# Performance work log

Measured on AMD Instinct MI355X. Metric: run time of the kernel, lower is better.

The kernel has to match this reference:

```python
import jax, jax.numpy as jnp
import numpy as np
from math import sqrt

B, S, I, H, O, R = 32, 2048, 128, 512, 64, 1
ALPHA = 0.1


def setup_inputs() -> dict:
    key = jax.random.key(0)
    ks = jax.random.split(key, 7)
    x = jax.random.normal(ks[0], (B, S, I), dtype=jnp.float32)
    input_projective = jax.random.normal(ks[1], (H, R), dtype=jnp.float32) / sqrt(H)
    input_receptive = jax.random.normal(ks[2], (I, R), dtype=jnp.float32) / sqrt(I)
    rec_projective = jax.random.normal(ks[3], (H, R), dtype=jnp.float32) / sqrt(H)
    rec_receptive = jax.random.normal(ks[4], (H, R), dtype=jnp.float32) / sqrt(H)
    bound = 1.0 / sqrt(H)
    readout_w = jax.random.uniform(ks[5], (O, H), minval=-bound, maxval=bound, dtype=jnp.float32)
    readout_b = jax.random.uniform(ks[6], (O,), minval=-bound, maxval=bound, dtype=jnp.float32)
    return {
        "x": x,
        "input_projective": input_projective,
        "input_receptive": input_receptive,
        "rec_projective": rec_projective,
        "rec_receptive": rec_receptive,
        "readout_w": readout_w,
        "readout_b": readout_b,
    }


def reference(x, input_projective, input_receptive, rec_projective, rec_receptive, readout_w, readout_b):
    # Precompute input drive for all steps using the low-rank factorization:
    # x_in[b,s,h] = x[b,s,:] @ input_receptive @ input_projective.T
    x_in = jnp.einsum("bsi,ir,hr->bsh", x, input_receptive, input_projective)

    def step(h, xin_t):
        # r_in = (J @ h.T).T with J = P @ R.T  ->  h @ R @ P.T (low-rank)
        r_in = (h @ rec_receptive) @ rec_projective.T
        dh = -h + jax.nn.relu(r_in + xin_t)  # activation = nlfun (relu)
        h = h + ALPHA * dh                   # Euler hidden update
        out_t = h @ readout_w.T + readout_b
        return h, out_t

    h0 = jnp.zeros((x.shape[0], rec_projective.shape[0]), dtype=x.dtype)
    _, out = jax.lax.scan(step, h0, jnp.swapaxes(x_in, 0, 1))  # scan over time
    return jnp.swapaxes(out, 0, 1)  # [B, S, O]
```

## Files before the change

### kernel.cpp

```cpp
#include <hip/hip_runtime.h>


#define B_ 32
#define S_ 2048
#define I_ 128
#define H_ 512
#define O_ 64

typedef __attribute__((ext_vector_type(8))) short bf16x8;
typedef __attribute__((ext_vector_type(4))) float f32x4;
typedef __attribute__((ext_vector_type(2))) float f32x2;

__device__ __forceinline__ unsigned short f2bf(float f) {
  unsigned int b = __float_as_uint(f);
  b += 0x7FFFu + ((b >> 16) & 1u);
  return (unsigned short)(b >> 16);
}
__device__ __forceinline__ float bf2f(unsigned short s) {
  return __uint_as_float(((unsigned)s) << 16);
}
__device__ __forceinline__ unsigned pack_bf(float lo, float hi) {
  unsigned a = (__float_as_uint(lo) + 0x8000u) >> 16;
  unsigned b = (__float_as_uint(hi) + 0x8000u) & 0xFFFF0000u;
  return a | b;
}

#define ROR_ADD(s, CTRL) \
  s += __int_as_float(__builtin_amdgcn_update_dpp(0, __float_as_int(s), CTRL, 0xF, 0xF, true))

#define RL(s, L) __int_as_float(__builtin_amdgcn_readlane(__float_as_int(s), (L)))

__device__ __forceinline__ void gload16(const void* g, void* l) {
  __builtin_amdgcn_global_load_lds(
      (const __attribute__((address_space(1))) unsigned int*)g,
      (__attribute__((address_space(3))) unsigned int*)l, 16, 0, 0);
}
#define WAITVM(N) asm volatile("s_waitcnt vmcnt(" #N ")" ::: "memory")

#define OFF_SU 0
#define OFF_SV 1920
#define OFF_RP 3456
#define OFF_IP 5504
#define OFF_SW 7552
#define OFF_XS 52608
#define SMEM_BYTES 150912

__device__ __forceinline__ int swz(int row, int col) {
  return row * 64 + (col ^ ((((unsigned)row >> 2) & 3) << 4));
}

__global__ __launch_bounds__(512, 1) void k_fused(
    const float* __restrict__ x, const float* __restrict__ ipj,
    const float* __restrict__ irc, const float* __restrict__ rpj,
    const float* __restrict__ rrc, const float* __restrict__ Wr,
    const float* __restrict__ bias, float* __restrict__ out) {
  extern __shared__ __align__(16) char smem[];
  float* su = (float*)(smem + OFF_SU);
  float* sV = (float*)(smem + OFF_SV);
  float* srp = (float*)(smem + OFF_RP);
  float* sip = (float*)(smem + OFF_IP);
  unsigned short* sw = (unsigned short*)(smem + OFF_SW);
  unsigned short* sBF = (unsigned short*)(smem + OFF_XS);
  float* xsf = (float*)(smem + OFF_XS);

  const int tid = threadIdx.x;
  const int wv = tid >> 6;
  const int lane = tid & 63;
  const int b = blockIdx.x >> 3;
  const int g = blockIdx.x & 7;
  const int r0 = g * 256;

  f32x4 cv0 = *(const f32x4*)(irc + 4 * (lane & 7));
  f32x4 cv1 = *(const f32x4*)(irc + 4 * (lane & 7) + 32);
  f32x4 cv2 = *(const f32x4*)(irc + 4 * (lane & 7) + 64);
  f32x4 cv3 = *(const f32x4*)(irc + 4 * (lane & 7) + 96);
  f32x2 a2[4], b2[4], lo2[4], hi2[4];
  #pragma unroll
  for (int k = 0; k < 4; k++) {
    float2 rp = ((const float2*)rpj)[lane + 64 * k];
    float2 ip = ((const float2*)ipj)[lane + 64 * k];
    float2 rr = ((const float2*)rrc)[lane + 64 * k];
    a2[k] = f32x2{0.1f * rr.x * rp.x, 0.1f * rr.y * rp.y};
    b2[k] = f32x2{0.1f * rr.x * ip.x, 0.1f * rr.y * ip.y};
    lo2[k] = f32x2{rr.x > 0.f ? 0.f : -__builtin_inff(),
                   rr.y > 0.f ? 0.f : -__builtin_inff()};
    hi2[k] = f32x2{rr.x > 0.f ? __builtin_inff() : 0.f,
                   rr.y > 0.f ? __builtin_inff() : 0.f};
  }
  if (tid < 32) { su[448 + tid] = 0.f; sV[352 + tid] = 0.f; }

#define ISSUE(c) do { \
    int tc_ = r0 - 192 + (c) * 64 + wv * 8; if (tc_ < 0) tc_ = 0; \
    const float* gs_ = x + ((size_t)b * S_ + tc_) * I_ + lane * 4; \
    char* ld_ = (char*)xsf + ((c) % 3) * 32768 + wv * 4096; \
    gload16(gs_,       ld_); \
    gload16(gs_ + 256, ld_ + 1024); \
    gload16(gs_ + 512, ld_ + 2048); \
    gload16(gs_ + 768, ld_ + 3072); \
  } while (0)

#define COMPUTE(c) do { \
    const float* bp_ = xsf + ((c) % 3) * 8192 + (wv * 8 + (lane >> 3)) * 128 + (lane & 7) * 4; \
    f32x4 x0_ = *(const f32x4*)(bp_); \
    f32x4 x1_ = *(const f32x4*)(bp_ + 32); \
    f32x4 x2_ = *(const f32x4*)(bp_ + 64); \
    f32x4 x3_ = *(const f32x4*)(bp_ + 96); \
    float p0_ = x0_[0] * cv0[0], p1_ = x0_[1] * cv0[1]; \
    float p2_ = x0_[2] * cv0[2], p3_ = x0_[3] * cv0[3]; \
    p0_ = fmaf(x1_[0], cv1[0], p0_); p1_ = fmaf(x1_[1], cv1[1], p1_); \
    p2_ = fmaf(x1_[2], cv1[2], p2_); p3_ = fmaf(x1_[3], cv1[3], p3_); \
    p0_ = fmaf(x2_[0], cv2[0], p0_); p1_ = fmaf(x2_[1], cv2[1], p1_); \
    p2_ = fmaf(x2_[2], cv2[2], p2_); p3_ = fmaf(x2_[3], cv2[3], p3_); \
    p0_ = fmaf(x3_[0], cv3[0], p0_); p1_ = fmaf(x3_[1], cv3[1], p1_); \
    p2_ = fmaf(x3_[2], cv3[2], p2_); p3_ = fmaf(x3_[3], cv3[3], p3_); \
    float s_ = (p0_ + p1_) + (p2_ + p3_); \
    ROR_ADD(s_, 0x121); ROR_ADD(s_, 0x122); ROR_ADD(s_, 0x124); \
    float mask_ = (r0 - 192 + (c) * 64 >= 0) ? 1.f : 0.f; \
    if ((lane & 7) == 7) su[(c) * 64 + wv * 8 + (lane >> 3)] = s_ * mask_; \
  } while (0)

  ISSUE(0); ISSUE(1); ISSUE(2);
  WAITVM(8); COMPUTE(0); ISSUE(3);
  WAITVM(8); COMPUTE(1); ISSUE(4);
  WAITVM(8); COMPUTE(2); ISSUE(5);
  WAITVM(8); COMPUTE(3); ISSUE(6);
  WAITVM(8); COMPUTE(4);
  WAITVM(4); COMPUTE(5);
  WAITVM(0); COMPUTE(6);
  __syncthreads();

  float4 wA0, wB0, wA1, wB1, wA2, wB2, wA3, wB3;
  float4 wA4, wB4, wA5, wB5, wA6, wB6, wA7, wB7;
#define WLOAD(m, A, Bv) do { \
    int seg_ = tid + 512 * (m); \
    int l2_ = seg_ & 63, ot_ = (seg_ >> 6) & 3, kt_ = seg_ >> 8; \
    const float4* wp_ = (const float4*)(Wr + (size_t)(ot_ * 16 + (l2_ & 15)) * H_ + kt_ * 32 + (l2_ >> 4) * 8); \
    A = wp_[0]; Bv = wp_[1]; \
  } while (0)
  WLOAD(0, wA0, wB0); WLOAD(1, wA1, wB1); WLOAD(2, wA2, wB2); WLOAD(3, wA3, wB3);
  WLOAD(4, wA4, wB4); WLOAD(5, wA5, wB5); WLOAD(6, wA6, wB6); WLOAD(7, wA7, wB7);
  float rpa = rpj[tid];
  float ipa = ipj[tid];

#define VSTEP(UT) do { \
    float ut_ = (UT); \
    f32x2 v2_ = {v, v}, u2_ = {ut_, ut_}; \
    f32x2 c0_ = __builtin_elementwise_min(__builtin_elementwise_max( \
        __builtin_elementwise_fma(v2_, a2[0], u2_ * b2[0]), lo2[0]), hi2[0]); \
    f32x2 c1_ = __builtin_elementwise_min(__builtin_elementwise_max( \
        __builtin_elementwise_fma(v2_, a2[1], u2_ * b2[1]), lo2[1]), hi2[1]); \
    f32x2 c2_ = __builtin_elementwise_min(__builtin_elementwise_max( \
        __builtin_elementwise_fma(v2_, a2[2], u2_ * b2[2]), lo2[2]), hi2[2]); \
    f32x2 c3_ = __builtin_elementwise_min(__builtin_elementwise_max( \
        __builtin_elementwise_fma(v2_, a2[3], u2_ * b2[3]), lo2[3]), hi2[3]); \
    f32x2 s2_ = (c0_ + c1_) + (c2_ + c3_); \
    float s_ = s2_[0] + s2_[1]; \
    ROR_ADD(s_, 0x121); ROR_ADD(s_, 0x122); ROR_ADD(s_, 0x124); ROR_ADD(s_, 0x128); \
    float tot_ = (RL(s_, 0) + RL(s_, 16)) + (RL(s_, 32) + RL(s_, 48)); \
    v = fmaf(0.9f, v, tot_); \
  } while (0)
  {
    float v = 0.f;
    int base = wv * 44;
    #pragma unroll 4
    for (int i = 0; i < 96; i++) VSTEP(su[base + i]);
    #pragma unroll 4
    for (int k = 0; k < 44; k++) {
      if (lane == 0) sV[base + k] = v;
      VSTEP(su[base + 96 + k]);
    }
  }

#define WPACK(m, A, Bv) do { \
    int seg_ = tid + 512 * (m); \
    uint4 pk_; \
    pk_.x = (unsigned)f2bf(A.x) | ((unsigned)f2bf(A.y) << 16); \
    pk_.y = (unsigned)f2bf(A.z) | ((unsigned)f2bf(A.w) << 16); \
    pk_.z = (unsigned)f2bf(Bv.x) | ((unsigned)f2bf(Bv.y) << 16); \
    pk_.w = (unsigned)f2bf(Bv.z) | ((unsigned)f2bf(Bv.w) << 16); \
    *(uint4*)(sBF + seg_ * 8) = pk_; \
  } while (0)
  WPACK(0, wA0, wB0); WPACK(1, wA1, wB1); WPACK(2, wA2, wB2); WPACK(3, wA3, wB3);
  WPACK(4, wA4, wB4); WPACK(5, wA5, wB5); WPACK(6, wA6, wB6); WPACK(7, wA7, wB7);
  srp[tid] = rpa;
  sip[tid] = ipa;
  __syncthreads();

  {
    int tl = lane & 15, quad = lane >> 4;
    float Vr0 = sV[(wv * 3 + 0) * 16 + tl], ur0 = su[96 + (wv * 3 + 0) * 16 + tl];
    float Vr1 = sV[(wv * 3 + 1) * 16 + tl], ur1 = su[96 + (wv * 3 + 1) * 16 + tl];
    float Vr2 = sV[(wv * 3 + 2) * 16 + tl], ur2 = su[96 + (wv * 3 + 2) * 16 + tl];
    f32x4 acc[3][4] = {};
    #pragma unroll 4
    for (int kt = 0; kt < 16; kt++) {
      int hbase = kt * 32 + quad * 8;
      f32x4 rp4a = *(const f32x4*)(srp + hbase);
      f32x4 rp4b = *(const f32x4*)(srp + hbase + 4);
      f32x4 ip4a = *(const f32x4*)(sip + hbase);
      f32x4 ip4b = *(const f32x4*)(sip + hbase + 4);
      bf16x8 bfr0 = *(const bf16x8*)(sBF + (((kt * 4 + 0) * 64 + lane) << 3));
      bf16x8 bfr1 = *(const bf16x8*)(sBF + (((kt * 4 + 1) * 64 + lane) << 3));
      bf16x8 bfr2 = *(const bf16x8*)(sBF + (((kt * 4 + 2) * 64 + lane) << 3));
      bf16x8 bfr3 = *(const bf16x8*)(sBF + (((kt * 4 + 3) * 64 + lane) << 3));
      #pragma unroll
      for (int m = 0; m < 3; m++) {
        float Vm = m == 0 ? Vr0 : (m == 1 ? Vr1 : Vr2);
        float um = m == 0 ? ur0 : (m == 1 ? ur1 : ur2);
        float q[8];
        #pragma unroll
        for (int j = 0; j < 4; j++) {
          q[j]     = fmaxf(fmaf(Vm, rp4a[j], um * ip4a[j]), 0.f);
          q[4 + j] = fmaxf(fmaf(Vm, rp4b[j], um * ip4b[j]), 0.f);
        }
        union { bf16x8 v; unsigned w[4]; } a;
        #pragma unroll
        for (int j = 0; j < 4; j++) a.w[j] = pack_bf(q[2 * j], q[2 * j + 1]);
        acc[m][0] = __builtin_amdgcn_mfma_f32_16x16x32_bf16(a.v, bfr0, acc[m][0], 0, 0, 0);
        acc[m][1] = __builtin_amdgcn_mfma_f32_16x16x32_bf16(a.v, bfr1, acc[m][1], 0, 0, 0);
        acc[m][2] = __builtin_amdgcn_mfma_f32_16x16x32_bf16(a.v, bfr2, acc[m][2], 0, 0, 0);
        acc[m][3] = __builtin_amdgcn_mfma_f32_16x16x32_bf16(a.v, bfr3, acc[m][3], 0, 0, 0);
      }
    }
    #pragma unroll
    for (int m = 0; m < 3; m++) {
      int mt = wv * 3 + m;
      if (mt < 22) {
        int rbase = mt * 16 + quad * 4;
        #pragma unroll
        for (int r = 0; r < 4; r++) {
          #pragma unroll
          for (int ot = 0; ot < 4; ot++)
            sw[swz(rbase + r, ot * 16 + tl)] = f2bf(acc[m][ot][r]);
        }
      }
    }
  }
  __syncthreads();

  {
    float y = 0.f;
    float bo = bias[lane];
    int k0 = wv * 32;
    float* ob = out + ((size_t)(b * S_ + r0 + k0)) * O_ + lane;
    #pragma unroll 8
    for (int i = 0; i < 96; i++)
      y = fmaf(0.9f, y, 0.1f * bf2f(sw[swz(k0 + i, lane)]));
    #pragma unroll 4
    for (int i = 0; i < 32; i++) {
      y = fmaf(0.9f, y, 0.1f * bf2f(sw[swz(k0 + 96 + i, lane)]));
      ob[(size_t)i * O_] = y + bo;
    }
  }
}

extern "C" void kernel_launch(void* const* d_in, const int* in_sizes, int n_in,
                              void* d_out, int out_size, void* d_ws, size_t ws_size,
                              hipStream_t stream) {
  const float* x   = (const float*)d_in[0];
  const float* ipj = (const float*)d_in[1];
  const float* irc = (const float*)d_in[2];
  const float* rpj = (const float*)d_in[3];
  const float* rrc = (const float*)d_in[4];
  const float* Wr  = (const float*)d_in[5];
  const float* br  = (const float*)d_in[6];
  float* out = (float*)d_out;

  static bool s_init = false;
  if (!s_init) {
    hipFuncSetAttribute((const void*)k_fused,
                        hipFuncAttributeMaxDynamicSharedMemorySize, SMEM_BYTES);
    s_init = true;
  }
  k_fused<<<dim3(256), dim3(512), SMEM_BYTES, stream>>>(x, ipj, irc, rpj, rrc,
                                                        Wr, br, out);
}
```

Measured before the change: 129.8 us.

## Double block to 1024 threads, halving per-wave work in every phase

After: 142.4 us. +9.7%, slower.

```diff
diff --git a/kernel.cpp b/kernel.cpp
--- a/kernel.cpp
+++ b/kernel.cpp
@@ -36,6 +36,7 @@
       (__attribute__((address_space(3))) unsigned int*)l, 16, 0, 0);
 }
 #define WAITVM(N) asm volatile("s_waitcnt vmcnt(" #N ")" ::: "memory")
+#define SCHEDB() __builtin_amdgcn_sched_barrier(0)
 
 #define OFF_SU 0
 #define OFF_SV 1920
@@ -49,7 +50,7 @@
   return row * 64 + (col ^ ((((unsigned)row >> 2) & 3) << 4));
 }
 
-__global__ __launch_bounds__(512, 1) void k_fused(
+__global__ __launch_bounds__(1024, 4) void k_fused(
     const float* __restrict__ x, const float* __restrict__ ipj,
     const float* __restrict__ irc, const float* __restrict__ rpj,
     const float* __restrict__ rrc, const float* __restrict__ Wr,
@@ -70,10 +71,8 @@
   const int g = blockIdx.x & 7;
   const int r0 = g * 256;
 
-  f32x4 cv0 = *(const f32x4*)(irc + 4 * (lane & 7));
-  f32x4 cv1 = *(const f32x4*)(irc + 4 * (lane & 7) + 32);
-  f32x4 cv2 = *(const f32x4*)(irc + 4 * (lane & 7) + 64);
-  f32x4 cv3 = *(const f32x4*)(irc + 4 * (lane & 7) + 96);
+  f32x4 cv0 = *(const f32x4*)(irc + 4 * (lane & 15));
+  f32x4 cv1 = *(const f32x4*)(irc + 64 + 4 * (lane & 15));
   f32x2 a2[4], b2[4], lo2[4], hi2[4];
   #pragma unroll
   for (int k = 0; k < 4; k++) {
@@ -90,57 +89,47 @@
   if (tid < 32) { su[448 + tid] = 0.f; sV[352 + tid] = 0.f; }
 
 #define ISSUE(c) do { \
-    int tc_ = r0 - 192 + (c) * 64 + wv * 8; if (tc_ < 0) tc_ = 0; \
+    int tc_ = r0 - 192 + (c) * 64 + wv * 4; if (tc_ < 0) tc_ = 0; \
     const float* gs_ = x + ((size_t)b * S_ + tc_) * I_ + lane * 4; \
-    char* ld_ = (char*)xsf + ((c) % 3) * 32768 + wv * 4096; \
+    char* ld_ = (char*)xsf + ((c) % 3) * 32768 + wv * 2048; \
     gload16(gs_,       ld_); \
     gload16(gs_ + 256, ld_ + 1024); \
-    gload16(gs_ + 512, ld_ + 2048); \
-    gload16(gs_ + 768, ld_ + 3072); \
   } while (0)
 
 #define COMPUTE(c) do { \
-    const float* bp_ = xsf + ((c) % 3) * 8192 + (wv * 8 + (lane >> 3)) * 128 + (lane & 7) * 4; \
+    const float* bp_ = xsf + ((c) % 3) * 8192 + (wv * 4 + (lane >> 4)) * 128 + (lane & 15) * 4; \
     f32x4 x0_ = *(const f32x4*)(bp_); \
-    f32x4 x1_ = *(const f32x4*)(bp_ + 32); \
-    f32x4 x2_ = *(const f32x4*)(bp_ + 64); \
-    f32x4 x3_ = *(const f32x4*)(bp_ + 96); \
+    f32x4 x1_ = *(const f32x4*)(bp_ + 64); \
     float p0_ = x0_[0] * cv0[0], p1_ = x0_[1] * cv0[1]; \
     float p2_ = x0_[2] * cv0[2], p3_ = x0_[3] * cv0[3]; \
     p0_ = fmaf(x1_[0], cv1[0], p0_); p1_ = fmaf(x1_[1], cv1[1], p1_); \
     p2_ = fmaf(x1_[2], cv1[2], p2_); p3_ = fmaf(x1_[3], cv1[3], p3_); \
-    p0_ = fmaf(x2_[0], cv2[0], p0_); p1_ = fmaf(x2_[1], cv2[1], p1_); \
-    p2_ = fmaf(x2_[2], cv2[2], p2_); p3_ = fmaf(x2_[3], cv2[3], p3_); \
-    p0_ = fmaf(x3_[0], cv3[0], p0_); p1_ = fmaf(x3_[1], cv3[1], p1_); \
-    p2_ = fmaf(x3_[2], cv3[2], p2_); p3_ = fmaf(x3_[3], cv3[3], p3_); \
     float s_ = (p0_ + p1_) + (p2_ + p3_); \
-    ROR_ADD(s_, 0x121); ROR_ADD(s_, 0x122); ROR_ADD(s_, 0x124); \
+    ROR_ADD(s_, 0x121); ROR_ADD(s_, 0x122); ROR_ADD(s_, 0x124); ROR_ADD(s_, 0x128); \
     float mask_ = (r0 - 192 + (c) * 64 >= 0) ? 1.f : 0.f; \
-    if ((lane & 7) == 7) su[(c) * 64 + wv * 8 + (lane >> 3)] = s_ * mask_; \
+    if ((lane & 15) == 0) su[(c) * 64 + wv * 4 + (lane >> 4)] = s_ * mask_; \
   } while (0)
 
   ISSUE(0); ISSUE(1); ISSUE(2);
-  WAITVM(8); COMPUTE(0); ISSUE(3);
-  WAITVM(8); COMPUTE(1); ISSUE(4);
-  WAITVM(8); COMPUTE(2); ISSUE(5);
-  WAITVM(8); COMPUTE(3); ISSUE(6);
-  WAITVM(8); COMPUTE(4);
-  WAITVM(4); COMPUTE(5);
+  WAITVM(4); COMPUTE(0); SCHEDB(); ISSUE(3);
+  WAITVM(4); COMPUTE(1); SCHEDB(); ISSUE(4);
+  WAITVM(4); COMPUTE(2); SCHEDB(); ISSUE(5);
+  WAITVM(4); COMPUTE(3); SCHEDB(); ISSUE(6);
+  WAITVM(4); COMPUTE(4);
+  WAITVM(2); COMPUTE(5);
   WAITVM(0); COMPUTE(6);
   __syncthreads();
 
   float4 wA0, wB0, wA1, wB1, wA2, wB2, wA3, wB3;
-  float4 wA4, wB4, wA5, wB5, wA6, wB6, wA7, wB7;
 #define WLOAD(m, A, Bv) do { \
-    int seg_ = tid + 512 * (m); \
+    int seg_ = tid + 1024 * (m); \
     int l2_ = seg_ & 63, ot_ = (seg_ >> 6) & 3, kt_ = seg_ >> 8; \
     const float4* wp_ = (const float4*)(Wr + (size_t)(ot_ * 16 + (l2_ & 15)) * H_ + kt_ * 32 + (l2_ >> 4) * 8); \
     A = wp_[0]; Bv = wp_[1]; \
   } while (0)
   WLOAD(0, wA0, wB0); WLOAD(1, wA1, wB1); WLOAD(2, wA2, wB2); WLOAD(3, wA3, wB3);
-  WLOAD(4, wA4, wB4); WLOAD(5, wA5, wB5); WLOAD(6, wA6, wB6); WLOAD(7, wA7, wB7);
-  float rpa = rpj[tid];
-  float ipa = ipj[tid];
+  float rpa = 0.f, ipa = 0.f;
+  if (tid < 512) { rpa = rpj[tid]; ipa = ipj[tid]; }
 
 #define VSTEP(UT) do { \
     float ut_ = (UT); \
@@ -161,18 +150,18 @@
   } while (0)
   {
     float v = 0.f;
-    int base = wv * 44;
+    int base = wv * 22;
     #pragma unroll 4
     for (int i = 0; i < 96; i++) VSTEP(su[base + i]);
-    #pragma unroll 4
-    for (int k = 0; k < 44; k++) {
+    #pragma unroll 2
+    for (int k = 0; k < 22; k++) {
       if (lane == 0) sV[base + k] = v;
       VSTEP(su[base + 96 + k]);
     }
   }
 
 #define WPACK(m, A, Bv) do { \
-    int seg_ = tid + 512 * (m); \
+    int seg_ = tid + 1024 * (m); \
     uint4 pk_; \
     pk_.x = (unsigned)f2bf(A.x) | ((unsigned)f2bf(A.y) << 16); \
     pk_.y = (unsigned)f2bf(A.z) | ((unsigned)f2bf(A.w) << 16); \
@@ -181,17 +170,17 @@
     *(uint4*)(sBF + seg_ * 8) = pk_; \
   } while (0)
   WPACK(0, wA0, wB0); WPACK(1, wA1, wB1); WPACK(2, wA2, wB2); WPACK(3, wA3, wB3);
-  WPACK(4, wA4, wB4); WPACK(5, wA5, wB5); WPACK(6, wA6, wB6); WPACK(7, wA7, wB7);
-  srp[tid] = rpa;
-  sip[tid] = ipa;
+  if (tid < 512) { srp[tid] = rpa; sip[tid] = ipa; }
   __syncthreads();
 
   {
     int tl = lane & 15, quad = lane >> 4;
-    float Vr0 = sV[(wv * 3 + 0) * 16 + tl], ur0 = su[96 + (wv * 3 + 0) * 16 + tl];
-    float Vr1 = sV[(wv * 3 + 1) * 16 + tl], ur1 = su[96 + (wv * 3 + 1) * 16 + tl];
-    float Vr2 = sV[(wv * 3 + 2) * 16 + tl], ur2 = su[96 + (wv * 3 + 2) * 16 + tl];
-    f32x4 acc[3][4] = {};
+    int mt0 = wv;
+    float Vr0 = sV[mt0 * 16 + tl], ur0 = su[96 + mt0 * 16 + tl];
+    float Vr1 = 0.f, ur1 = 0.f;
+    if (wv < 6) { Vr1 = sV[(16 + wv) * 16 + tl]; ur1 = su[96 + (16 + wv) * 16 + tl]; }
+    f32x4 acc0[4] = {};
+    f32x4 acc1[4] = {};
     #pragma unroll 4
     for (int kt = 0; kt < 16; kt++) {
       int hbase = kt * 32 + quad * 8;
@@ -203,36 +192,53 @@
       bf16x8 bfr1 = *(const bf16x8*)(sBF + (((kt * 4 + 1) * 64 + lane) << 3));
       bf16x8 bfr2 = *(const bf16x8*)(sBF + (((kt * 4 + 2) * 64 + lane) << 3));
       bf16x8 bfr3 = *(const bf16x8*)(sBF + (((kt * 4 + 3) * 64 + lane) << 3));
-      #pragma unroll
-      for (int m = 0; m < 3; m++) {
-        float Vm = m == 0 ? Vr0 : (m == 1 ? Vr1 : Vr2);
-        float um = m == 0 ? ur0 : (m == 1 ? ur1 : ur2);
+      {
         float q[8];
         #pragma unroll
         for (int j = 0; j < 4; j++) {
-          q[j]     = fmaxf(fmaf(Vm, rp4a[j], um * ip4a[j]), 0.f);
-          q[4 + j] = fmaxf(fmaf(Vm, rp4b[j], um * ip4b[j]), 0.f);
+          q[j]     = fmaxf(fmaf(Vr0, rp4a[j], ur0 * ip4a[j]), 0.f);
+          q[4 + j] = fmaxf(fmaf(Vr0, rp4b[j], ur0 * ip4b[j]), 0.f);
         }
         union { bf16x8 v; unsigned w[4]; } a;
         #pragma unroll
         for (int j = 0; j < 4; j++) a.w[j] = pack_bf(q[2 * j], q[2 * j + 1]);
-        acc[m][0] = __builtin_amdgcn_mfma_f32_16x16x32_bf16(a.v, bfr0, acc[m][0], 0, 0, 0);
-        acc[m][1] = __builtin_amdgcn_mfma_f32_16x16x32_bf16(a.v, bfr1, acc[m][1], 0, 0, 0);
-        acc[m][2] = __builtin_amdgcn_mfma_f32_16x16x32_bf16(a.v, bfr2, acc[m][2], 0, 0, 0);
-        acc[m][3] = __builtin_amdgcn_mfma_f32_16x16x32_bf16(a.v, bfr3, acc[m][3], 0, 0, 0);
-      }
-    }
-    #pragma unroll
-    for (int m = 0; m < 3; m++) {
-      int mt = wv * 3 + m;
-      if (mt < 22) {
-        int rbase = mt * 16 + quad * 4;
-        #pragma unroll
-        for (int r = 0; r < 4; r++) {
-          #pragma unroll
-          for (int ot = 0; ot < 4; ot++)
-            sw[swz(rbase + r, ot * 16 + tl)] = f2bf(acc[m][ot][r]);
+        acc0[0] = __builtin_amdgcn_mfma_f32_16x16x32_bf16(a.v, bfr0, acc0[0], 0, 0, 0);
+        acc0[1] = __builtin_amdgcn_mfma_f32_16x16x32_bf16(a.v, bfr1, acc0[1], 0, 0, 0);
+        acc0[2] = __builtin_amdgcn_mfma_f32_16x16x32_bf16(a.v, bfr2, acc0[2], 0, 0, 0);
+        acc0[3] = __builtin_amdgcn_mfma_f32_16x16x32_bf16(a.v, bfr3, acc0[3], 0, 0, 0);
+      }
+      if (wv < 6) {
+        float q[8];
+        #pragma unroll
+        for (int j = 0; j < 4; j++) {
+          q[j]     = fmaxf(fmaf(Vr1, rp4a[j], ur1 * ip4a[j]), 0.f);
+          q[4 + j] = fmaxf(fmaf(Vr1, rp4b[j], ur1 * ip4b[j]), 0.f);
         }
+        union { bf16x8 v; unsigned w[4]; } a;
+        #pragma unroll
+        for (int j = 0; j < 4; j++) a.w[j] = pack_bf(q[2 * j], q[2 * j + 1]);
+        acc1[0] = __builtin_amdgcn_mfma_f32_16x16x32_bf16(a.v, bfr0, acc1[0], 0, 0, 0);
+        acc1[1] = __builtin_amdgcn_mfma_f32_16x16x32_bf16(a.v, bfr1, acc1[1], 0, 0, 0);
+        acc1[2] = __builtin_amdgcn_mfma_f32_16x16x32_bf16(a.v, bfr2, acc1[2], 0, 0, 0);
+        acc1[3] = __builtin_amdgcn_mfma_f32_16x16x32_bf16(a.v, bfr3, acc1[3], 0, 0, 0);
+      }
+    }
+    {
+      int rbase = mt0 * 16 + quad * 4;
+      #pragma unroll
+      for (int r = 0; r < 4; r++) {
+        #pragma unroll
+        for (int ot = 0; ot < 4; ot++)
+          sw[swz(rbase + r, ot * 16 + tl)] = f2bf(acc0[ot][r]);
+      }
+    }
+    if (wv < 6) {
+      int rbase = (16 + wv) * 16 + quad * 4;
+      #pragma unroll
+      for (int r = 0; r < 4; r++) {
+        #pragma unroll
+        for (int ot = 0; ot < 4; ot++)
+          sw[swz(rbase + r, ot * 16 + tl)] = f2bf(acc1[ot][r]);
       }
     }
   }
@@ -241,13 +247,13 @@
   {
     float y = 0.f;
     float bo = bias[lane];
-    int k0 = wv * 32;
+    int k0 = wv * 16;
     float* ob = out + ((size_t)(b * S_ + r0 + k0)) * O_ + lane;
     #pragma unroll 8
     for (int i = 0; i < 96; i++)
       y = fmaf(0.9f, y, 0.1f * bf2f(sw[swz(k0 + i, lane)]));
     #pragma unroll 4
-    for (int i = 0; i < 32; i++) {
+    for (int i = 0; i < 16; i++) {
       y = fmaf(0.9f, y, 0.1f * bf2f(sw[swz(k0 + 96 + i, lane)]));
       ob[(size_t)i * O_] = y + bo;
     }
@@ -272,6 +278,6 @@
                         hipFuncAttributeMaxDynamicSharedMemorySize, SMEM_BYTES);
     s_init = true;
   }
-  k_fused<<<dim3(256), dim3(512), SMEM_BYTES, stream>>>(x, ipj, irc, rpj, rrc,
-                                                        Wr, br, out);
-}
+  k_fused<<<dim3(256), dim3(1024), SMEM_BYTES, stream>>>(x, ipj, irc, rpj, rrc,
+                                                         Wr, br, out);
+}
```
